# Kernel tuning notes

Hardware: AMD Instinct MI355X
Metric: run time of the kernel (lower is better)

## Reference

```python
import jax, jax.numpy as jnp
import numpy as np

NUM_PATCHES = 128  # static stand-in for max(patch_ids)+1


def setup_inputs() -> dict:
    key = jax.random.key(0)
    k1, k2, k3, k4 = jax.random.split(key, 4)
    B, S, H, D = 8, 8192, 512, 768
    byte_hiddens = jax.random.normal(k1, (B, S, H), dtype=jnp.float32)
    patch_ids = jnp.sort(jax.random.randint(k2, (B, S), 0, NUM_PATCHES), axis=-1)
    # Dense output_projection (glorot-uniform-ish init)
    lim = float(np.sqrt(6.0 / (H + D)))
    W_proj = jax.random.uniform(k3, (H, D), minval=-lim, maxval=lim, dtype=jnp.float32)
    b_proj = jnp.zeros((D,), dtype=jnp.float32)
    return {"byte_hiddens": byte_hiddens, "W_proj": W_proj, "b_proj": b_proj,
            "patch_ids": patch_ids}


def reference(byte_hiddens, W_proj, b_proj, patch_ids):
    # Mean pooling within patches: for each patch p, mean of byte_hiddens where
    # patch_ids == p (sum / max(count, 1)), then Dense projection.
    B, S, H = byte_hiddens.shape
    P = NUM_PATCHES
    # Flatten batch into segment ids so one segment_sum covers all (b, p) pairs.
    seg = (patch_ids + jnp.arange(B, dtype=patch_ids.dtype)[:, None] * P).reshape(-1)
    flat = byte_hiddens.reshape(B * S, H)
    sums = jax.ops.segment_sum(flat, seg, num_segments=B * P)          # [B*P, H]
    counts = jax.ops.segment_sum(jnp.ones((B * S,), byte_hiddens.dtype), seg,
                                 num_segments=B * P)                   # [B*P]
    means = sums / jnp.maximum(counts, 1.0)[:, None]                   # [B*P, H]
    means = means.reshape(B, P, H)
    return means @ W_proj + b_proj                                     # [B, P, D]
```

## Files before the change

### kernel.cpp

```cpp
#include <hip/hip_runtime.h>

#define B_ 8
#define S_ 8192
#define H_ 512
#define D_ 768
#define P_ 128

__global__ __launch_bounds__(128) void bounds_kernel(
    const int* __restrict__ ids, int* __restrict__ bounds)
{
    const int b = blockIdx.x;
    const int p = threadIdx.x;
    const int* row = ids + (size_t)b * S_;
    int lo = 0, hi = S_;
    #pragma unroll 13
    while (lo < hi) { int mid = (lo + hi) >> 1; if (row[mid] < p) lo = mid + 1; else hi = mid; }
    bounds[b * (P_ + 1) + p] = lo;
    if (p == 0) bounds[b * (P_ + 1) + P_] = S_;
}

__global__ __launch_bounds__(256) void pool_kernel(
    const float* __restrict__ bh, const int* __restrict__ bounds,
    float* __restrict__ means)
{
    const int p = blockIdx.x;
    const int b = blockIdx.y;
    const int t = threadIdx.x;
    const int c = t & 127;
    const int r_ofs = t >> 7;

    const int start = bounds[b * (P_ + 1) + p];
    const int end   = bounds[b * (P_ + 1) + p + 1];
    const int cnt   = end - start;

    const float4* src = (const float4*)(bh + ((size_t)b * S_ + (size_t)start) * H_) + c;
    float4 a0 = {0.f, 0.f, 0.f, 0.f};
    float4 a1 = {0.f, 0.f, 0.f, 0.f};

    int r = r_ofs;
    for (; r + 2 < cnt; r += 4) {
        float4 v0 = src[(size_t)r * (H_ / 4)];
        float4 v1 = src[(size_t)(r + 2) * (H_ / 4)];
        a0.x += v0.x; a0.y += v0.y; a0.z += v0.z; a0.w += v0.w;
        a1.x += v1.x; a1.y += v1.y; a1.z += v1.z; a1.w += v1.w;
    }
    if (r < cnt) {
        float4 v = src[(size_t)r * (H_ / 4)];
        a0.x += v.x; a0.y += v.y; a0.z += v.z; a0.w += v.w;
    }
    float4 s;
    s.x = a0.x + a1.x; s.y = a0.y + a1.y; s.z = a0.z + a1.z; s.w = a0.w + a1.w;

    __shared__ float4 red[128];
    if (r_ofs == 1) red[c] = s;
    __syncthreads();
    if (r_ofs == 0) {
        float4 o = red[c];
        const float inv = 1.0f / (float)(cnt > 0 ? cnt : 1);
        float4 out;
        out.x = (s.x + o.x) * inv; out.y = (s.y + o.y) * inv;
        out.z = (s.z + o.z) * inv; out.w = (s.w + o.w) * inv;
        ((float4*)(means + ((size_t)(b * P_ + p)) * H_))[c] = out;
    }
}

__global__ __launch_bounds__(256) void gemm_kernel(
    const float* __restrict__ A, const float* __restrict__ W,
    const float* __restrict__ bias, float* __restrict__ C)
{
    const int K = H_, N = D_;
    __shared__ float As[16][68];
    __shared__ float Bs[16][64];

    const int t  = threadIdx.x;
    const int tx = t & 15;
    const int ty = t >> 4;
    const int m0 = blockIdx.y * 64;
    const int n0 = blockIdx.x * 64;

    const int am = t >> 2;
    const int ak = (t & 3) * 4;
    const int bk = t >> 4;
    const int bn = (t & 15) * 4;
    const float* Aptr = A + (size_t)(m0 + am) * K + ak;
    const float* Wptr = W + (size_t)bk * N + (n0 + bn);

    float4 a_reg = *(const float4*)Aptr;
    float4 b_reg = *(const float4*)Wptr;

    float acc[4][4] = {};

    for (int k0 = 0; k0 < K; k0 += 16) {
        As[ak + 0][am] = a_reg.x;
        As[ak + 1][am] = a_reg.y;
        As[ak + 2][am] = a_reg.z;
        As[ak + 3][am] = a_reg.w;
        *(float4*)&Bs[bk][bn] = b_reg;
        __syncthreads();

        if (k0 + 16 < K) {
            a_reg = *(const float4*)(Aptr + (k0 + 16));
            b_reg = *(const float4*)(Wptr + (size_t)(k0 + 16) * N);
        }

        #pragma unroll
        for (int k = 0; k < 16; ++k) {
            float4 a4 = *(const float4*)&As[k][ty * 4];
            float4 b4 = *(const float4*)&Bs[k][tx * 4];
            const float a[4] = {a4.x, a4.y, a4.z, a4.w};
            const float bb[4] = {b4.x, b4.y, b4.z, b4.w};
            #pragma unroll
            for (int i = 0; i < 4; ++i)
                #pragma unroll
                for (int j = 0; j < 4; ++j)
                    acc[i][j] += a[i] * bb[j];
        }
        __syncthreads();
    }

    const float4 bv = *(const float4*)&bias[n0 + tx * 4];
    const float badd[4] = {bv.x, bv.y, bv.z, bv.w};
    #pragma unroll
    for (int i = 0; i < 4; ++i) {
        const int m = m0 + ty * 4 + i;
        float4 o;
        o.x = acc[i][0] + badd[0];
        o.y = acc[i][1] + badd[1];
        o.z = acc[i][2] + badd[2];
        o.w = acc[i][3] + badd[3];
        *(float4*)&C[(size_t)m * N + n0 + tx * 4] = o;
    }
}

extern "C" void kernel_launch(void* const* d_in, const int* in_sizes, int n_in,
                              void* d_out, int out_size, void* d_ws, size_t ws_size,
                              hipStream_t stream) {
    const float* bh   = (const float*)d_in[0];
    const float* W    = (const float*)d_in[1];
    const float* bias = (const float*)d_in[2];
    const int*   ids  = (const int*)d_in[3];
    float* out   = (float*)d_out;
    float* means = (float*)d_ws;
    int*   bounds = (int*)(means + (size_t)B_ * P_ * H_);

    bounds_kernel<<<dim3(B_), 128, 0, stream>>>(ids, bounds);

    dim3 g1(P_, B_);
    pool_kernel<<<g1, 256, 0, stream>>>(bh, bounds, means);

    dim3 g2(D_ / 64, (B_ * P_) / 64);
    gemm_kernel<<<g2, 256, 0, stream>>>(means, W, bias, out);
}
```

Before: 229.1 us.

## Use bf16 MFMA GEMM, fold bounds search into pooling, pre-transpose weights

Replaces the fp32 SIMT GEMM with a bf16 MFMA 16x16x32 GEMM. Means are stored as bf16 and the weights are converted and transposed to bf16 by a new kernel. The separate bounds kernel is removed and each pooling block does two binary searches itself to find its segment. The GEMM is small next to the memory-bound pooling pass over 128MB, so the overall gain is likely modest, and bf16 lowers precision.

```diff
diff --git a/kernel.cpp b/kernel.cpp
--- a/kernel.cpp
+++ b/kernel.cpp
@@ -6,22 +6,54 @@
 #define D_ 768
 #define P_ 128
 
-__global__ __launch_bounds__(128) void bounds_kernel(
-    const int* __restrict__ ids, int* __restrict__ bounds)
+typedef __attribute__((ext_vector_type(8))) short bf16x8;
+typedef __attribute__((ext_vector_type(4))) float f32x4;
+
+static __device__ inline unsigned short f2bf(float f) {
+    unsigned int u = __float_as_uint(f);
+    unsigned int r = (u + 0x7fffu + ((u >> 16) & 1u)) >> 16;
+    return (unsigned short)r;
+}
+
+
+__global__ __launch_bounds__(256) void wt_kernel(
+    const float* __restrict__ W, unsigned short* __restrict__ Wt)
 {
-    const int b = blockIdx.x;
-    const int p = threadIdx.x;
-    const int* row = ids + (size_t)b * S_;
-    int lo = 0, hi = S_;
-    #pragma unroll 13
-    while (lo < hi) { int mid = (lo + hi) >> 1; if (row[mid] < p) lo = mid + 1; else hi = mid; }
-    bounds[b * (P_ + 1) + p] = lo;
-    if (p == 0) bounds[b * (P_ + 1) + P_] = S_;
+    const int nb = blockIdx.x * 64;
+    const int kb = blockIdx.y * 64;
+    __shared__ unsigned short T[64][72];
+    const int t = threadIdx.x;
+    {
+        const int kk = t >> 4;
+        const int nn = (t & 15) * 4;
+        #pragma unroll
+        for (int i = 0; i < 4; ++i) {
+            float4 v = *(const float4*)&W[(size_t)(kb + kk + i * 16) * D_ + nb + nn];
+            T[nn + 0][kk + i * 16] = f2bf(v.x);
+            T[nn + 1][kk + i * 16] = f2bf(v.y);
+            T[nn + 2][kk + i * 16] = f2bf(v.z);
+            T[nn + 3][kk + i * 16] = f2bf(v.w);
+        }
+    }
+    __syncthreads();
+    {
+        const int nn = t >> 4;
+        const int kk = (t & 15) * 4;
+        #pragma unroll
+        for (int i = 0; i < 4; ++i) {
+            ushort4 o;
+            o.x = T[nn + i * 16][kk + 0];
+            o.y = T[nn + i * 16][kk + 1];
+            o.z = T[nn + i * 16][kk + 2];
+            o.w = T[nn + i * 16][kk + 3];
+            *(ushort4*)&Wt[(size_t)(nb + nn + i * 16) * H_ + kb + kk] = o;
+        }
+    }
 }
 
 __global__ __launch_bounds__(256) void pool_kernel(
-    const float* __restrict__ bh, const int* __restrict__ bounds,
-    float* __restrict__ means)
+    const float* __restrict__ bh, const int* __restrict__ ids,
+    unsigned short* __restrict__ means)
 {
     const int p = blockIdx.x;
     const int b = blockIdx.y;
@@ -29,14 +61,21 @@
     const int c = t & 127;
     const int r_ofs = t >> 7;
 
-    const int start = bounds[b * (P_ + 1) + p];
-    const int end   = bounds[b * (P_ + 1) + p + 1];
-    const int cnt   = end - start;
+    const int* row = ids + (size_t)b * S_;
+    int lo0 = 0, hi0 = S_, lo1 = 0, hi1 = S_;
+    #pragma unroll
+    for (int it = 0; it < 13; ++it) {
+        int m0 = (lo0 + hi0) >> 1, m1 = (lo1 + hi1) >> 1;
+        int v0 = row[m0], v1 = row[m1];
+        if (v0 < p)  lo0 = m0 + 1; else hi0 = m0;
+        if (v1 <= p) lo1 = m1 + 1; else hi1 = m1;
+    }
+    const int start = lo0;
+    const int cnt   = lo1 - lo0;
 
     const float4* src = (const float4*)(bh + ((size_t)b * S_ + (size_t)start) * H_) + c;
     float4 a0 = {0.f, 0.f, 0.f, 0.f};
     float4 a1 = {0.f, 0.f, 0.f, 0.f};
-
     int r = r_ofs;
     for (; r + 2 < cnt; r += 4) {
         float4 v0 = src[(size_t)r * (H_ / 4)];
@@ -57,78 +96,73 @@
     if (r_ofs == 0) {
         float4 o = red[c];
         const float inv = 1.0f / (float)(cnt > 0 ? cnt : 1);
-        float4 out;
-        out.x = (s.x + o.x) * inv; out.y = (s.y + o.y) * inv;
-        out.z = (s.z + o.z) * inv; out.w = (s.w + o.w) * inv;
-        ((float4*)(means + ((size_t)(b * P_ + p)) * H_))[c] = out;
+        ushort4 w;
+        w.x = f2bf((s.x + o.x) * inv);
+        w.y = f2bf((s.y + o.y) * inv);
+        w.z = f2bf((s.z + o.z) * inv);
+        w.w = f2bf((s.w + o.w) * inv);
+        *(ushort4*)&means[((size_t)(b * P_ + p)) * H_ + c * 4] = w;
     }
 }
 
 __global__ __launch_bounds__(256) void gemm_kernel(
-    const float* __restrict__ A, const float* __restrict__ W,
+    const unsigned short* __restrict__ A, const unsigned short* __restrict__ Bt,
     const float* __restrict__ bias, float* __restrict__ C)
 {
-    const int K = H_, N = D_;
-    __shared__ float As[16][68];
-    __shared__ float Bs[16][64];
+    __shared__ unsigned short As[64][40];
+    __shared__ unsigned short Bs[64][40];
 
-    const int t  = threadIdx.x;
-    const int tx = t & 15;
-    const int ty = t >> 4;
-    const int m0 = blockIdx.y * 64;
-    const int n0 = blockIdx.x * 64;
+    const int t    = threadIdx.x;
+    const int lane = t & 63;
+    const int wv   = t >> 6;
+    const int mrow = lane & 15;
+    const int quad = lane >> 4;
+    const int m0   = blockIdx.y * 64;
+    const int n0   = blockIdx.x * 64;
 
-    const int am = t >> 2;
-    const int ak = (t & 3) * 4;
-    const int bk = t >> 4;
-    const int bn = (t & 15) * 4;
-    const float* Aptr = A + (size_t)(m0 + am) * K + ak;
-    const float* Wptr = W + (size_t)bk * N + (n0 + bn);
+    const int sr = t >> 2;
+    const int sk = (t & 3) * 8;
+    const unsigned short* Aptr = A  + (size_t)(m0 + sr) * H_ + sk;
+    const unsigned short* Bptr = Bt + (size_t)(n0 + sr) * H_ + sk;
 
-    float4 a_reg = *(const float4*)Aptr;
-    float4 b_reg = *(const float4*)Wptr;
+    uint4 a_reg = *(const uint4*)Aptr;
+    uint4 b_reg = *(const uint4*)Bptr;
 
-    float acc[4][4] = {};
+    f32x4 acc[4] = {};
 
-    for (int k0 = 0; k0 < K; k0 += 16) {
-        As[ak + 0][am] = a_reg.x;
-        As[ak + 1][am] = a_reg.y;
-        As[ak + 2][am] = a_reg.z;
-        As[ak + 3][am] = a_reg.w;
-        *(float4*)&Bs[bk][bn] = b_reg;
+    for (int k0 = 0; k0 < H_; k0 += 32) {
+        *(uint4*)&As[sr][sk] = a_reg;
+        *(uint4*)&Bs[sr][sk] = b_reg;
         __syncthreads();
 
-        if (k0 + 16 < K) {
-            a_reg = *(const float4*)(Aptr + (k0 + 16));
-            b_reg = *(const float4*)(Wptr + (size_t)(k0 + 16) * N);
+        if (k0 + 32 < H_) {
+            a_reg = *(const uint4*)(Aptr + k0 + 32);
+            b_reg = *(const uint4*)(Bptr + k0 + 32);
         }
 
         #pragma unroll
-        for (int k = 0; k < 16; ++k) {
-            float4 a4 = *(const float4*)&As[k][ty * 4];
-            float4 b4 = *(const float4*)&Bs[k][tx * 4];
-            const float a[4] = {a4.x, a4.y, a4.z, a4.w};
-            const float bb[4] = {b4.x, b4.y, b4.z, b4.w};
+        for (int kk = 0; kk < 2; ++kk) {
+        }
+        {
+            bf16x8 af = *(const bf16x8*)&As[wv * 16 + mrow][quad * 8];
             #pragma unroll
-            for (int i = 0; i < 4; ++i)
-                #pragma unroll
-                for (int j = 0; j < 4; ++j)
-                    acc[i][j] += a[i] * bb[j];
+            for (int t4 = 0; t4 < 4; ++t4) {
+                bf16x8 bf = *(const bf16x8*)&Bs[t4 * 16 + mrow][quad * 8];
+                acc[t4] = __builtin_amdgcn_mfma_f32_16x16x32_bf16(af, bf, acc[t4], 0, 0, 0);
+            }
         }
         __syncthreads();
     }
 
-    const float4 bv = *(const float4*)&bias[n0 + tx * 4];
-    const float badd[4] = {bv.x, bv.y, bv.z, bv.w};
     #pragma unroll
-    for (int i = 0; i < 4; ++i) {
-        const int m = m0 + ty * 4 + i;
-        float4 o;
-        o.x = acc[i][0] + badd[0];
-        o.y = acc[i][1] + badd[1];
-        o.z = acc[i][2] + badd[2];
-        o.w = acc[i][3] + badd[3];
-        *(float4*)&C[(size_t)m * N + n0 + tx * 4] = o;
+    for (int t4 = 0; t4 < 4; ++t4) {
+        const int col = n0 + t4 * 16 + mrow;
+        const float bia = bias[col];
+        #pragma unroll
+        for (int r = 0; r < 4; ++r) {
+            const int rowi = m0 + wv * 16 + quad * 4 + r;
+            C[(size_t)rowi * D_ + col] = acc[t4][r] + bia;
+        }
     }
 }
 
@@ -139,15 +173,13 @@
     const float* W    = (const float*)d_in[1];
     const float* bias = (const float*)d_in[2];
     const int*   ids  = (const int*)d_in[3];
-    float* out   = (float*)d_out;
-    float* means = (float*)d_ws;
-    int*   bounds = (int*)(means + (size_t)B_ * P_ * H_);
+    float* out = (float*)d_out;
 
-    bounds_kernel<<<dim3(B_), 128, 0, stream>>>(ids, bounds);
+    unsigned short* means = (unsigned short*)d_ws;
+    unsigned short* Wt    = means + (size_t)B_ * P_ * H_;
 
-    dim3 g1(P_, B_);
-    pool_kernel<<<g1, 256, 0, stream>>>(bh, bounds, means);
-
-    dim3 g2(D_ / 64, (B_ * P_) / 64);
-    gemm_kernel<<<g2, 256, 0, stream>>>(means, W, bias, out);
+    wt_kernel<<<dim3(D_ / 64, H_ / 64), 256, 0, stream>>>(W, Wt);
+    pool_kernel<<<dim3(P_, B_), 256, 0, stream>>>(bh, ids, means);
+    gemm_kernel<<<dim3(D_ / 64, (B_ * P_) / 64), 256, 0, stream>>>(
+        means, Wt, bias, out);
 }
```

New measurement: 210.2 us. -8.2%, faster.
